# Kernel tuning notes

Hardware: AMD Instinct MI355X
Metric: run time of the kernel (lower is better)

The kernel has to match this reference:

```python
import jax, jax.numpy as jnp
import numpy as np

B, N, D_MODEL = 4, 4096, 1024
HEADS, DIM_HEAD = 8, 64
INNER = HEADS * DIM_HEAD  # 512
NB_FEAT = int(DIM_HEAD * np.log(DIM_HEAD))  # 266, performer default
D_FF = 4 * D_MODEL
KERNEL_EPS = 1e-4
LN_EPS = 1e-5


def setup_inputs() -> dict:
    key = jax.random.key(0)
    ks = jax.random.split(key, 12)
    w = lambda i, shape: jax.random.normal(ks[i], shape, jnp.float32) * 0.02
    z = lambda *shape: jnp.zeros(shape, jnp.float32)
    o = lambda *shape: jnp.ones(shape, jnp.float32)
    return dict(
        x=jax.random.normal(ks[0], (B, N, D_MODEL), jnp.float32),
        proj_w=w(1, (D_MODEL, D_MODEL)), proj_b=z(D_MODEL),
        ln1_g=o(D_MODEL), ln1_b=z(D_MODEL),
        wq=w(2, (D_MODEL, INNER)), bq=z(INNER),
        wk=w(3, (D_MODEL, INNER)), bk=z(INNER),
        wv=w(4, (D_MODEL, INNER)), bv=z(INNER),
        wo=w(5, (INNER, D_MODEL)), bo=z(D_MODEL),
        proj_mat=jax.random.normal(ks[6], (NB_FEAT, DIM_HEAD), jnp.float32),
        ln2_g=o(D_MODEL), ln2_b=z(D_MODEL),
        w1=w(7, (D_MODEL, D_FF)), b1=z(D_FF),
        w2=w(8, (D_FF, D_MODEL)), b2=z(D_MODEL),
    )


def _layer_norm(x, g, b):
    mu = x.mean(-1, keepdims=True)
    var = ((x - mu) ** 2).mean(-1, keepdims=True)
    return (x - mu) * jax.lax.rsqrt(var + LN_EPS) * g + b


def _softmax_kernel(data, proj_mat, is_query):
    # data: [b,h,n,d], proj_mat: [m,d] -> features [b,h,n,m]
    dn = DIM_HEAD ** -0.25            # data_normalizer
    ratio = NB_FEAT ** -0.5
    dd = jnp.einsum('bhnd,md->bhnm', data * dn, proj_mat)
    diag = (data ** 2).sum(-1, keepdims=True) * (0.5 * dn * dn)
    if is_query:
        mx = dd.max(-1, keepdims=True)
    else:
        mx = dd.max(axis=(-1, -2), keepdims=True)
    return ratio * (jnp.exp(dd - diag - mx) + KERNEL_EPS)


def _favor_attention(q, k, v, proj_mat):
    # non-causal FAVOR+ linear attention; q,k,v: [b,h,n,d]
    qp = _softmax_kernel(q, proj_mat, True)    # [b,h,n,m]
    kp = _softmax_kernel(k, proj_mat, False)   # [b,h,n,m]
    k_sum = kp.sum(-2)                         # [b,h,m]
    d_inv = 1.0 / jnp.einsum('bhnm,bhm->bhn', qp, k_sum)
    ctx = jnp.einsum('bhnm,bhnd->bhmd', kp, v)
    return jnp.einsum('bhmd,bhnm,bhn->bhnd', ctx, qp, d_inv)


def _performer(x, ln1_g, ln1_b, wq, bq, wk, bk, wv, bv, wo, bo, proj_mat,
               ln2_g, ln2_b, w1, b1, w2, b2):
    # pre-norm self-attention block
    h = _layer_norm(x, ln1_g, ln1_b)
    split = lambda t: t.reshape(B, N, HEADS, DIM_HEAD).transpose(0, 2, 1, 3)
    q = split(h @ wq + bq)
    k = split(h @ wk + bk)
    v = split(h @ wv + bv)
    attn = _favor_attention(q, k, v, proj_mat)
    attn = attn.transpose(0, 2, 1, 3).reshape(B, N, INNER)
    x = x + attn @ wo + bo
    # pre-norm feed-forward block
    h = _layer_norm(x, ln2_g, ln2_b)
    x = x + jax.nn.gelu(h @ w1 + b1, approximate=False) @ w2 + b2
    return x


def reference(x, proj_w, proj_b, ln1_g, ln1_b, wq, bq, wk, bk, wv, bv,
              wo, bo, proj_mat, ln2_g, ln2_b, w1, b1, w2, b2):
    u = x @ proj_w + proj_b                    # dense gate branch
    v = _performer(x, ln1_g, ln1_b, wq, bq, wk, bk, wv, bv, wo, bo,
                   proj_mat, ln2_g, ln2_b, w1, b1, w2, b2)
    return u * v
```

## Files before the change

kernel.cpp:

```cpp
#include <hip/hip_runtime.h>
#include <math.h>

typedef unsigned short bf16_t;
using bf16x8 = __attribute__((ext_vector_type(8))) short;
using f32x4  = __attribute__((ext_vector_type(4))) float;

#define DEVFN static __device__ __forceinline__

DEVFN float b2f(bf16_t u){ unsigned v=((unsigned)u)<<16; float f; __builtin_memcpy(&f,&v,4); return f; }
DEVFN bf16_t f2b(float f){ unsigned u; __builtin_memcpy(&u,&f,4); u += 0x7fffu + ((u>>16)&1u); return (bf16_t)(u>>16); }
DEVFN unsigned encf(float f){ unsigned u=__float_as_uint(f); return (u&0x80000000u)? ~u : (u|0x80000000u); }
DEVFN float decf(unsigned e){ return __uint_as_float((e&0x80000000u)? (e^0x80000000u) : ~e); }

DEVFN float erf_fast(float x){
  float ax = fabsf(x);
  float t = __builtin_amdgcn_rcpf(1.0f + 0.3275911f*ax);
  float y = t*(0.254829592f + t*(-0.284496736f + t*(1.421413741f
          + t*(-1.453152027f + t*1.061405429f))));
  float r = 1.0f - y*__expf(-ax*ax);
  return copysignf(r, x);
}

constexpr float DN_SCALE = 0.35355339059327373f;
constexpr float RATIO    = 0.06131393394849658f;
constexpr float KEPS     = 1e-4f;
#define MPAD 288

#define GLOAD_LDS16(g, l) __builtin_amdgcn_global_load_lds( \
    (__attribute__((address_space(1))) void*)(g), \
    (__attribute__((address_space(3))) void*)(l), 16, 0, 0)

#define MFMA16(a,b,c) __builtin_amdgcn_mfma_f32_16x16x32_bf16(a,b,c,0,0,0)

DEVFN void hard_barrier(){
  __builtin_amdgcn_sched_barrier(0);
  asm volatile("s_barrier" ::: "memory");
  __builtin_amdgcn_sched_barrier(0);
}
#define WAITVM(N) asm volatile("s_waitcnt vmcnt(" #N ")" ::: "memory")

__global__ __launch_bounds__(256)
void wt_cast(const float* __restrict__ W, bf16_t* __restrict__ Wt, int K, int N)
{
  __shared__ alignas(16) float ts[32][33];
  int t = threadIdx.x;
  int r = t>>3, c4 = (t&7)*4;
  int k0 = blockIdx.x*32, n0 = blockIdx.y*32;
  float4 v = *(const float4*)(W + (size_t)(k0+r)*N + n0 + c4);
  ts[r][c4+0]=v.x; ts[r][c4+1]=v.y; ts[r][c4+2]=v.z; ts[r][c4+3]=v.w;
  __syncthreads();
  ushort4 o;
  o.x = f2b(ts[c4+0][r]); o.y = f2b(ts[c4+1][r]);
  o.z = f2b(ts[c4+2][r]); o.w = f2b(ts[c4+3][r]);
  *(ushort4*)(Wt + (size_t)(n0+r)*K + k0 + c4) = o;
}

__global__ __launch_bounds__(256)
void concat_bias(const float* __restrict__ bq, const float* __restrict__ bk,
                 const float* __restrict__ bv, float* __restrict__ dst)
{
  int t = blockIdx.x*256 + threadIdx.x;
  if (t < 512) dst[t] = bq[t];
  else if (t < 1024) dst[t] = bk[t-512];
  else dst[t] = bv[t-1024];
}

__global__ void mx_init(unsigned* m){ if (threadIdx.x < 32) m[threadIdx.x] = 0u; }

__global__ void zero_out(float* o, long n){
  long i = (long)blockIdx.x*256 + threadIdx.x;
  if (i < n) o[i] = 0.f;
}

__global__ __launch_bounds__(256)
void pm_cast(const float* __restrict__ pm, bf16_t* __restrict__ pmb)
{
  int idx = blockIdx.x*256 + threadIdx.x;
  int r = idx>>6, c = idx&63;
  pmb[idx] = (r < 266) ? f2b(pm[r*64+c]*DN_SCALE) : (bf16_t)0;
}

__global__ __launch_bounds__(256)
void vt_trans(const bf16_t* __restrict__ qkv, bf16_t* __restrict__ vT)
{
  __shared__ ushort ts[32][36];
  int by = blockIdx.y;
  int bh = by>>1, dt = by&1, b = bh>>3, h = bh&7;
  int n0 = blockIdx.x*32;
  int t = threadIdx.x, r = t>>3, c4 = (t&7)*4;
  ushort4 v = *(const ushort4*)(qkv + ((size_t)b*4096 + n0 + r)*1536 + 1024 + h*64 + dt*32 + c4);
  ts[r][c4+0]=v.x; ts[r][c4+1]=v.y; ts[r][c4+2]=v.z; ts[r][c4+3]=v.w;
  __syncthreads();
  ushort4 o;
  o.x = ts[c4+0][r]; o.y = ts[c4+1][r]; o.z = ts[c4+2][r]; o.w = ts[c4+3][r];
  *(ushort4*)(vT + ((size_t)bh*64 + dt*32 + r)*4096 + n0 + c4) = o;
}

__global__ __launch_bounds__(256)
void ln_kernel(const float* __restrict__ x, const float* __restrict__ g,
               const float* __restrict__ b, bf16_t* __restrict__ out)
{
  long row = blockIdx.x; int t = threadIdx.x;
  float4 v = ((const float4*)x)[row*256 + t];
  float s = v.x+v.y+v.z+v.w;
  #pragma unroll
  for (int o=32;o>0;o>>=1) s += __shfl_xor(s, o);
  __shared__ float r1[4], r2[4];
  if ((t&63)==0) r1[t>>6] = s;
  __syncthreads();
  float mu = (r1[0]+r1[1]+r1[2]+r1[3]) * (1.f/1024.f);
  float dx = v.x-mu, dy = v.y-mu, dz = v.z-mu, dw = v.w-mu;
  float ss = dx*dx+dy*dy+dz*dz+dw*dw;
  #pragma unroll
  for (int o=32;o>0;o>>=1) ss += __shfl_xor(ss, o);
  if ((t&63)==0) r2[t>>6] = ss;
  __syncthreads();
  float var = (r2[0]+r2[1]+r2[2]+r2[3]) * (1.f/1024.f);
  float rs = rsqrtf(var + 1e-5f);
  float4 gg = ((const float4*)g)[t], bb = ((const float4*)b)[t];
  ushort4 o4;
  o4.x = f2b(dx*rs*gg.x+bb.x); o4.y = f2b(dy*rs*gg.y+bb.y);
  o4.z = f2b(dz*rs*gg.z+bb.z); o4.w = f2b(dw*rs*gg.w+bb.w);
  ((ushort4*)out)[row*256+t] = o4;
}

__global__ __launch_bounds__(256)
void cast_f32_bf16(const float* __restrict__ in, bf16_t* __restrict__ out)
{
  long i = (long)blockIdx.x*256 + threadIdx.x;
  float4 v = ((const float4*)in)[i];
  ushort4 o;
  o.x = f2b(v.x); o.y = f2b(v.y); o.z = f2b(v.z); o.w = f2b(v.w);
  ((ushort4*)out)[i] = o;
}

template<int RES, int GELU, int GATEF, int OBF>
__global__ __launch_bounds__(256)
void gemm_bt(const bf16_t* __restrict__ A, int lda,
             const bf16_t* __restrict__ Bt, int ldb,
             const float* __restrict__ bias,
             const float* res,
             const float* gatef,
             void* Cout, int N, int K)
{
  __shared__ alignas(16) bf16_t As[3][128*32];
  __shared__ alignas(16) bf16_t Bs[3][128*32];
  const int tid = threadIdx.x;
  const int wid = tid>>6, lane = tid&63;
  const int l15 = lane&15, l4 = lane>>4;
  const int wm = wid>>1, wn = wid&1;

  const int NX = gridDim.x;
  const int nwg = NX * gridDim.y;
  const int lid = blockIdx.y*NX + blockIdx.x;
  const int qc = nwg>>3;
  const int wgid = (lid&7)*qc + (lid>>3);
  const int stripe = wgid / (16*NX);
  const int rem    = wgid % (16*NX);
  const long m0 = (long)(stripe*16 + (rem & 15))*128;
  const long n0 = (long)(rem >> 4)*128;

  f32x4 acc[4][4];
  #pragma unroll
  for (int i=0;i<4;i++)
    #pragma unroll
    for (int j=0;j<4;j++) acc[i][j] = f32x4{0.f,0.f,0.f,0.f};

  const bf16_t* ga = A  + (size_t)(m0 + (tid>>2))*lda + (tid&3)*8;
  const bf16_t* gb = Bt + (size_t)(n0 + (tid>>2))*ldb + (tid&3)*8;

  auto STAGE = [&](bf16_t* Ab, bf16_t* Bb){
    GLOAD_LDS16(ga,                   Ab + wid*512);
    GLOAD_LDS16(ga + (size_t)64*lda,  Ab + 2048 + wid*512);
    GLOAD_LDS16(gb,                   Bb + wid*512);
    GLOAD_LDS16(gb + (size_t)64*ldb,  Bb + 2048 + wid*512);
    ga += 32; gb += 32;
  };

  const int nt = K >> 5;
  STAGE(As[0], Bs[0]);
  STAGE(As[1], Bs[1]);
  int i0 = 0, i1 = 1, i2 = 2;
  for (int t = 0; t < nt; ++t){
    if (t+2 < nt){ STAGE(As[i2], Bs[i2]); WAITVM(8); }
    else if (t+1 < nt){ WAITVM(4); }
    else { WAITVM(0); }
    hard_barrier();
    const bf16_t* Ab = As[i0];
    const bf16_t* Bb = Bs[i0];
    bf16x8 af[4], bfr[4];
    #pragma unroll
    for (int i=0;i<4;i++){
      af[i]  = *(const bf16x8*)(Ab + (wm*64 + i*16 + l15)*32 + l4*8);
      bfr[i] = *(const bf16x8*)(Bb + (wn*64 + i*16 + l15)*32 + l4*8);
    }
    #pragma unroll
    for (int i=0;i<4;i++)
      #pragma unroll
      for (int j=0;j<4;j++)
        acc[i][j] = MFMA16(af[i], bfr[j], acc[i][j]);
    hard_barrier();
    int tmp = i0; i0 = i1; i1 = i2; i2 = tmp;
  }

  #pragma unroll
  for (int i=0;i<4;i++){
    #pragma unroll
    for (int j=0;j<4;j++){
      #pragma unroll
      for (int r=0;r<4;r++){
        long row = m0 + wm*64 + i*16 + l4*4 + r;
        long col = n0 + wn*64 + j*16 + l15;
        float v = acc[i][j][r] + bias[col];
        if constexpr (RES)   v += res[row*(long)N + col];
        if constexpr (GELU)  v = 0.5f*v*(1.0f + erf_fast(v*0.70710678118654752f));
        if constexpr (GATEF) v *= gatef[row*(long)N + col];
        if constexpr (OBF)  ((bf16_t*)Cout)[row*(long)N + col] = f2b(v);
        else                ((float* )Cout)[row*(long)N + col] = v;
      }
    }
  }
}


__global__ __launch_bounds__(256,2)
void favor_kmax2(const bf16_t* __restrict__ qkv, const bf16_t* __restrict__ pmb,
                 unsigned* __restrict__ mxk)
{
  int bh = blockIdx.y, b = bh>>3, h = bh&7;
  int t = threadIdx.x, wid = t>>6, lane = t&63;
  int l15 = lane&15, l4 = lane>>4;
  int n0 = blockIdx.x*64, row0 = wid*16;
  f32x4 acc[18];
  #pragma unroll
  for (int c=0;c<18;c++) acc[c] = f32x4{0.f,0.f,0.f,0.f};
  const bf16_t* abase = qkv + ((size_t)(b*4096) + n0 + row0 + l15)*1536 + 512 + h*64;
  #pragma unroll
  for (int kh=0;kh<2;kh++){
    bf16x8 a = *(const bf16x8*)(abase + kh*32 + l4*8);
    #pragma unroll
    for (int ct=0;ct<18;ct++){
      bf16x8 bb = *(const bf16x8*)(pmb + (ct*16+l15)*64 + kh*32 + l4*8);
      acc[ct] = MFMA16(a, bb, acc[ct]);
    }
  }
  float mx = -3e38f;
  #pragma unroll
  for (int ct=0;ct<18;ct++){
    if (ct*16 + l15 < 266){
      #pragma unroll
      for (int r=0;r<4;r++) mx = fmaxf(mx, acc[ct][r]);
    }
  }
  #pragma unroll
  for (int o=32;o>0;o>>=1) mx = fmaxf(mx, __shfl_xor(mx, o));
  __shared__ float red[4];
  if (lane==0) red[wid] = mx;
  __syncthreads();
  if (t==0){
    float m2 = fmaxf(fmaxf(red[0],red[1]),fmaxf(red[2],red[3]));
    atomicMax(mxk + bh, encf(m2));
  }
}

__global__ __launch_bounds__(256,2)
void favor_kp(const bf16_t* __restrict__ qkv, const bf16_t* __restrict__ pmb,
              const unsigned* __restrict__ mxk, bf16_t* __restrict__ kpT, int bh0)
{
  int bhl = blockIdx.y, bh = bh0 + bhl, b = bh>>3, h = bh&7;
  int t = threadIdx.x, wid = t>>6, lane = t&63;
  int l15 = lane&15, l4 = lane>>4;
  int n0 = blockIdx.x*64, row0 = wid*16;
  f32x4 acc[18];
  #pragma unroll
  for (int c=0;c<18;c++) acc[c] = f32x4{0.f,0.f,0.f,0.f};
  const bf16_t* abase = qkv + ((size_t)(b*4096) + n0 + row0 + l15)*1536 + 512 + h*64;
  float rsq = 0.f;
  #pragma unroll
  for (int kh=0;kh<2;kh++){
    bf16x8 a = *(const bf16x8*)(abase + kh*32 + l4*8);
    #pragma unroll
    for (int e=0;e<8;e++){ float v = b2f((bf16_t)a[e]); rsq += v*v; }
    #pragma unroll
    for (int ct=0;ct<18;ct++){
      bf16x8 bb = *(const bf16x8*)(pmb + (ct*16+l15)*64 + kh*32 + l4*8);
      acc[ct] = MFMA16(a, bb, acc[ct]);
    }
  }
  rsq += __shfl_xor(rsq, 16);
  rsq += __shfl_xor(rsq, 32);
  float MX = decf(mxk[bh]);
  constexpr float DSC = 0.5f*DN_SCALE*DN_SCALE;
  float dg[4];
  #pragma unroll
  for (int r=0;r<4;r++) dg[r] = DSC * __shfl(rsq, l4*4 + r);
  #pragma unroll
  for (int ct=0;ct<18;ct++){
    int col = ct*16 + l15;
    ushort4 o;
    if (col < 266){
      o.x = f2b(RATIO*(__expf(acc[ct][0] - dg[0] - MX) + KEPS));
      o.y = f2b(RATIO*(__expf(acc[ct][1] - dg[1] - MX) + KEPS));
      o.z = f2b(RATIO*(__expf(acc[ct][2] - dg[2] - MX) + KEPS));
      o.w = f2b(RATIO*(__expf(acc[ct][3] - dg[3] - MX) + KEPS));
    } else { o.x=0; o.y=0; o.z=0; o.w=0; }
    *(ushort4*)(kpT + ((size_t)bhl*MPAD + col)*4096 + n0 + row0 + l4*4) = o;
  }
}

__global__ __launch_bounds__(256)
void ksum_kernel(const bf16_t* __restrict__ kpT, float* __restrict__ ksumf, int bh0)
{
  int t = threadIdx.x, wid = t>>6, lane = t&63;
  int rr = blockIdx.x*4 + wid;
  int bhl = rr/272, m = rr%272;
  const bf16_t* row = kpT + ((size_t)bhl*MPAD + m)*4096;
  float s = 0.f;
  #pragma unroll
  for (int j=0;j<8;j++){
    bf16x8 v = *(const bf16x8*)(row + j*512 + lane*8);
    #pragma unroll
    for (int e=0;e<8;e++) s += b2f((bf16_t)v[e]);
  }
  #pragma unroll
  for (int o=32;o>0;o>>=1) s += __shfl_xor(s, o);
  if (lane==0) ksumf[(size_t)(bh0+bhl)*MPAD + m] = s;
}

__global__ __launch_bounds__(256,2)
void ctx_gemm(const bf16_t* __restrict__ kpT, const bf16_t* __restrict__ vT,
              float* __restrict__ ctxP, int bh0)
{
  int m0 = blockIdx.x*16, ks = blockIdx.y, bhl = blockIdx.z, bh = bh0 + bhl;
  int t = threadIdx.x, wid = t>>6, lane = t&63;
  int l15 = lane&15, l4 = lane>>4;
  f32x4 acc[4];
  #pragma unroll
  for (int c=0;c<4;c++) acc[c] = f32x4{0.f,0.f,0.f,0.f};
  const bf16_t* Abase = kpT + ((size_t)bhl*MPAD + m0 + l15)*4096;
  const bf16_t* Bbase = vT + ((size_t)bh*64)*4096;
  const int kb = ks*1024 + wid*256;
  for (int k = kb; k < kb + 256; k += 32){
    bf16x8 a = *(const bf16x8*)(Abase + k + l4*8);
    #pragma unroll
    for (int ct=0;ct<4;ct++){
      bf16x8 bb = *(const bf16x8*)(Bbase + (size_t)(ct*16+l15)*4096 + k + l4*8);
      acc[ct] = MFMA16(a, bb, acc[ct]);
    }
  }
  __shared__ float red[4][4][16][16];
  #pragma unroll
  for (int ct=0;ct<4;ct++)
    #pragma unroll
    for (int r=0;r<4;r++) red[wid][ct][l4*4+r][l15] = acc[ct][r];
  __syncthreads();
  #pragma unroll
  for (int i=0;i<4;i++){
    int e = i*256 + t;
    int ct = e>>8, row = (e>>4)&15, col = e&15;
    float s = ((red[0][ct][row][col] + red[1][ct][row][col])
             + (red[2][ct][row][col] + red[3][ct][row][col]));
    ctxP[(((size_t)bhl*4 + ks)*272 + m0 + row)*64 + ct*16 + col] = s;
  }
}

__global__ __launch_bounds__(256)
void ctx_reduce(const float* __restrict__ ctxP, bf16_t* __restrict__ ctxT, int bh0)
{
  int bhl = blockIdx.y, bh = bh0 + bhl;
  int idx = blockIdx.x*256 + threadIdx.x;
  int m = idx>>6, d = idx&63;
  float s = 0.f;
  if (m < 272){
    #pragma unroll
    for (int ks=0;ks<4;ks++)
      s += ctxP[(((size_t)bhl*4 + ks)*272 + m)*64 + d];
  }
  ctxT[((size_t)bh*64 + d)*MPAD + m] = f2b(s);
}

__global__ __launch_bounds__(256,2)
void favor_q(const bf16_t* __restrict__ qkv, const bf16_t* __restrict__ pmb,
             const float* __restrict__ ksumf,
             const bf16_t* __restrict__ ctxT, bf16_t* __restrict__ attn)
{
  __shared__ alignas(16) ushort qpLds[64*296];
  __shared__ float ksLds[288];
  int bh = blockIdx.y, b = bh>>3, h = bh&7;
  int t = threadIdx.x, wid = t>>6, lane = t&63;
  int l15 = lane&15, l4 = lane>>4;
  int n0 = blockIdx.x*64, row0 = wid*16;
  ksLds[t] = ksumf[(size_t)bh*MPAD + t];
  if (t < 32) ksLds[256+t] = ksumf[(size_t)bh*MPAD + 256 + t];
  __syncthreads();

  f32x4 acc[18];
  #pragma unroll
  for (int c=0;c<18;c++) acc[c] = f32x4{0.f,0.f,0.f,0.f};
  const bf16_t* abase = qkv + ((size_t)(b*4096) + n0 + row0 + l15)*1536 + h*64;
  float rsq = 0.f;
  #pragma unroll
  for (int kh=0;kh<2;kh++){
    bf16x8 a = *(const bf16x8*)(abase + kh*32 + l4*8);
    #pragma unroll
    for (int e=0;e<8;e++){ float v = b2f((bf16_t)a[e]); rsq += v*v; }
    #pragma unroll
    for (int ct=0;ct<18;ct++){
      bf16x8 bb = *(const bf16x8*)(pmb + (ct*16+l15)*64 + kh*32 + l4*8);
      acc[ct] = MFMA16(a, bb, acc[ct]);
    }
  }
  rsq += __shfl_xor(rsq, 16);
  rsq += __shfl_xor(rsq, 32);
  constexpr float DSC = 0.5f*DN_SCALE*DN_SCALE;
  float dg[4];
  #pragma unroll
  for (int r=0;r<4;r++) dg[r] = DSC * __shfl(rsq, l4*4 + r);

  float mxr[4] = {-3e38f,-3e38f,-3e38f,-3e38f};
  #pragma unroll
  for (int ct=0;ct<18;ct++){
    if (ct*16 + l15 < 266){
      #pragma unroll
      for (int r=0;r<4;r++) mxr[r] = fmaxf(mxr[r], acc[ct][r]);
    }
  }
  #pragma unroll
  for (int r=0;r<4;r++){
    mxr[r] = fmaxf(mxr[r], __shfl_xor(mxr[r], 1));
    mxr[r] = fmaxf(mxr[r], __shfl_xor(mxr[r], 2));
    mxr[r] = fmaxf(mxr[r], __shfl_xor(mxr[r], 4));
    mxr[r] = fmaxf(mxr[r], __shfl_xor(mxr[r], 8));
  }
  float den[4] = {0.f,0.f,0.f,0.f};
  #pragma unroll
  for (int ct=0;ct<18;ct++){
    int col = ct*16 + l15;
    float ks = ksLds[col];
    #pragma unroll
    for (int r=0;r<4;r++){
      float qpv = 0.f;
      if (col < 266){
        qpv = RATIO*(__expf(acc[ct][r] - dg[r] - mxr[r]) + KEPS);
        den[r] += qpv*ks;
      }
      qpLds[(row0 + l4*4 + r)*296 + col] = f2b(qpv);
    }
  }
  float dinv[4];
  #pragma unroll
  for (int r=0;r<4;r++){
    den[r] += __shfl_xor(den[r], 1);
    den[r] += __shfl_xor(den[r], 2);
    den[r] += __shfl_xor(den[r], 4);
    den[r] += __shfl_xor(den[r], 8);
    dinv[r] = 1.0f/den[r];
  }
  __syncthreads();

  f32x4 o2[4];
  #pragma unroll
  for (int c=0;c<4;c++) o2[c] = f32x4{0.f,0.f,0.f,0.f};
  const bf16_t* Bbase = ctxT + (size_t)bh*64*MPAD;
  #pragma unroll
  for (int kk=0;kk<9;kk++){
    int k0 = kk*32;
    bf16x8 a = *(const bf16x8*)&qpLds[(row0 + l15)*296 + k0 + l4*8];
    #pragma unroll
    for (int ct=0;ct<4;ct++){
      bf16x8 bb = *(const bf16x8*)(Bbase + (size_t)(ct*16+l15)*MPAD + k0 + l4*8);
      o2[ct] = MFMA16(a, bb, o2[ct]);
    }
  }
  #pragma unroll
  for (int ct=0;ct<4;ct++)
    #pragma unroll
    for (int r=0;r<4;r++)
      attn[((size_t)(b*4096) + n0 + row0 + l4*4 + r)*512 + h*64 + ct*16 + l15]
        = f2b(o2[ct][r] * dinv[r]);
}

extern "C" void kernel_launch(void* const* d_in, const int* in_sizes, int n_in,
                              void* d_out, int out_size, void* d_ws, size_t ws_size,
                              hipStream_t stream)
{
  (void)in_sizes; (void)n_in; (void)out_size;
  const float* x      = (const float*)d_in[0];
  const float* proj_w = (const float*)d_in[1];
  const float* proj_b = (const float*)d_in[2];
  const float* ln1_g  = (const float*)d_in[3];
  const float* ln1_b  = (const float*)d_in[4];
  const float* wq     = (const float*)d_in[5];
  const float* bq     = (const float*)d_in[6];
  const float* wk     = (const float*)d_in[7];
  const float* bk     = (const float*)d_in[8];
  const float* wv     = (const float*)d_in[9];
  const float* bv     = (const float*)d_in[10];
  const float* wo     = (const float*)d_in[11];
  const float* bo     = (const float*)d_in[12];
  const float* pm     = (const float*)d_in[13];
  const float* ln2_g  = (const float*)d_in[14];
  const float* ln2_b  = (const float*)d_in[15];
  const float* w1     = (const float*)d_in[16];
  const float* b1     = (const float*)d_in[17];
  const float* w2     = (const float*)d_in[18];
  const float* b2     = (const float*)d_in[19];
  float* out = (float*)d_out;
  const size_t MB = 1ull<<20;

  char* ws = (char*)d_ws;
  size_t off = 0;
  auto alloc = [&](size_t bytes)->void*{ void* p = ws + off; off += (bytes + 255) & ~(size_t)255; return p; };
  bf16_t* Wt_proj = (bf16_t*)alloc(2ul*1024*1024);
  bf16_t* Wt_qkv  = (bf16_t*)alloc(2ul*1536*1024);
  bf16_t* Wt_o    = (bf16_t*)alloc(2ul*1024*512);
  bf16_t* Wt_1    = (bf16_t*)alloc(2ul*4096*1024);
  bf16_t* Wt_2    = (bf16_t*)alloc(2ul*1024*4096);
  float*  bqkv    = (float*) alloc(4ul*1536);
  unsigned* mxk   = (unsigned*)alloc(4ul*32);
  bf16_t* pmb     = (bf16_t*)alloc(2ul*MPAD*64);
  float*  ksumf   = (float*) alloc(4ul*32*MPAD);
  bf16_t* ctxT    = (bf16_t*)alloc(2ul*32*64*MPAD);
  float*  ctxP    = (float*) alloc(4ul*8*4*272*64);
  char*   R       = (char*)  alloc(0);
  size_t R_avail = (ws_size > off) ? ws_size - off : 0;

  if (R_avail < 67*MB){ zero_out<<<dim3(65536), 256, 0, stream>>>(out, 16777216L); return; }
  int KG = (R_avail >= 87*MB) ? 8 : 4;
  int NC = (R_avail >= 84*MB) ? 2 : 4;

  bf16_t* qkv  = (bf16_t*)(R);
  bf16_t* h1c  = (bf16_t*)(R + 48*MB);
  bf16_t* kpT  = (bf16_t*)(R + 48*MB);
  bf16_t* attn = (bf16_t*)(R + 48*MB);
  long    CH   = 16384/NC;
  bf16_t* h2c  = (bf16_t*)(R);
  bf16_t* ff1c = (bf16_t*)(R + 16*MB);
  bf16_t* vT   = (bf16_t*)d_out;

  wt_cast<<<dim3(32,32), 256, 0, stream>>>(proj_w, Wt_proj, 1024, 1024);
  wt_cast<<<dim3(32,16), 256, 0, stream>>>(wq, Wt_qkv,              1024, 512);
  wt_cast<<<dim3(32,16), 256, 0, stream>>>(wk, Wt_qkv + 512*1024,   1024, 512);
  wt_cast<<<dim3(32,16), 256, 0, stream>>>(wv, Wt_qkv + 1024*1024,  1024, 512);
  wt_cast<<<dim3(16,32), 256, 0, stream>>>(wo, Wt_o, 512, 1024);
  wt_cast<<<dim3(32,128),256, 0, stream>>>(w1, Wt_1, 1024, 4096);
  wt_cast<<<dim3(128,32),256, 0, stream>>>(w2, Wt_2, 4096, 1024);
  concat_bias<<<dim3(6), 256, 0, stream>>>(bq, bk, bv, bqkv);
  pm_cast<<<dim3(72), 256, 0, stream>>>(pm, pmb);

  for (int c = 0; c < 2; c++){
    ln_kernel<<<dim3(8192), 256, 0, stream>>>(x + (size_t)c*8192*1024, ln1_g, ln1_b, h1c);
    gemm_bt<0,0,0,1><<<dim3(12,64), 256, 0, stream>>>(h1c, 1024, Wt_qkv, 1024,
        bqkv, nullptr, nullptr, qkv + (size_t)c*8192*1536, 1536, 1024);
  }

  vt_trans<<<dim3(128,64), 256, 0, stream>>>(qkv, vT);
  mx_init<<<dim3(1), 64, 0, stream>>>(mxk);
  favor_kmax2<<<dim3(64,32), 256, 0, stream>>>(qkv, pmb, mxk);
  for (int g = 0; g < 32; g += KG){
    favor_kp<<<dim3(64,KG), 256, 0, stream>>>(qkv, pmb, mxk, kpT, g);
    ksum_kernel<<<dim3(KG*68), 256, 0, stream>>>(kpT, ksumf, g);
    ctx_gemm<<<dim3(17,4,KG), 256, 0, stream>>>(kpT, vT, ctxP, g);
    ctx_reduce<<<dim3(72,KG), 256, 0, stream>>>(ctxP, ctxT, g);
  }
  favor_q<<<dim3(64,32), 256, 0, stream>>>(qkv, pmb, ksumf, ctxT, attn);

  gemm_bt<1,0,0,0><<<dim3(8,128), 256, 0, stream>>>(attn, 512, Wt_o, 512,
      bo, x, nullptr, out, 1024, 512);

  for (int c = 0; c < NC; c++){
    float* xrow = out + (size_t)c*CH*1024;
    ln_kernel<<<dim3((unsigned)CH), 256, 0, stream>>>(xrow, ln2_g, ln2_b, h2c);
    gemm_bt<0,1,0,1><<<dim3(32,(unsigned)(CH/128)), 256, 0, stream>>>(h2c, 1024, Wt_1, 1024,
        b1, nullptr, nullptr, ff1c, 4096, 1024);
    gemm_bt<1,0,0,0><<<dim3(8,(unsigned)(CH/128)), 256, 0, stream>>>(ff1c, 4096, Wt_2, 4096,
        b2, xrow, nullptr, xrow, 1024, 4096);
    cast_f32_bf16<<<dim3((unsigned)CH), 256, 0, stream>>>(x + (size_t)c*CH*1024, h2c);
    gemm_bt<0,0,1,0><<<dim3(8,(unsigned)(CH/128)), 256, 0, stream>>>(h2c, 1024, Wt_proj, 1024,
        proj_b, nullptr, xrow, xrow, 1024, 1024);
  }
}
```

Baseline: 1.032 ms.

## Fuse k_sum into ctx_gemm and use one barrier per GEMM k-step

Removes the separate ksum_kernel by accumulating the per-feature sums of the bf16 kp rows inside ctx_gemm as the A fragments are loaded, then reducing the partial sums in ctx_reduce. This saves one extra read of kpT and a kernel launch per group. It also changes the GEMM main loop to wait and barrier once per step, issuing the next stage's async loads after that barrier instead of before it. Dropping the trailing barrier relies on the triple-buffer rotation to avoid overwriting LDS that other waves are still reading. The favor_q load of ksumf now guards against entries past 272.

Result: no change. 1.020 ms (-1.1%).

```diff
diff --git a/kernel.cpp b/kernel.cpp
--- a/kernel.cpp
+++ b/kernel.cpp
@@ -32,12 +32,8 @@
 
 #define MFMA16(a,b,c) __builtin_amdgcn_mfma_f32_16x16x32_bf16(a,b,c,0,0,0)
 
-DEVFN void hard_barrier(){
-  __builtin_amdgcn_sched_barrier(0);
-  asm volatile("s_barrier" ::: "memory");
-  __builtin_amdgcn_sched_barrier(0);
-}
 #define WAITVM(N) asm volatile("s_waitcnt vmcnt(" #N ")" ::: "memory")
+#define RAW_BARRIER() asm volatile("s_barrier" ::: "memory")
 
 __global__ __launch_bounds__(256)
 void wt_cast(const float* __restrict__ W, bf16_t* __restrict__ Wt, int K, int N)
@@ -182,10 +178,10 @@
   STAGE(As[1], Bs[1]);
   int i0 = 0, i1 = 1, i2 = 2;
   for (int t = 0; t < nt; ++t){
-    if (t+2 < nt){ STAGE(As[i2], Bs[i2]); WAITVM(8); }
-    else if (t+1 < nt){ WAITVM(4); }
-    else { WAITVM(0); }
-    hard_barrier();
+    if (t < nt-1) { WAITVM(4); }
+    else          { WAITVM(0); }
+    RAW_BARRIER();
+    if (t+2 < nt) STAGE(As[i2], Bs[i2]);
     const bf16_t* Ab = As[i0];
     const bf16_t* Bb = Bs[i0];
     bf16x8 af[4], bfr[4];
@@ -199,7 +195,6 @@
       #pragma unroll
       for (int j=0;j<4;j++)
         acc[i][j] = MFMA16(af[i], bfr[j], acc[i][j]);
-    hard_barrier();
     int tmp = i0; i0 = i1; i1 = i2; i2 = tmp;
   }
 
@@ -308,28 +303,9 @@
   }
 }
 
-__global__ __launch_bounds__(256)
-void ksum_kernel(const bf16_t* __restrict__ kpT, float* __restrict__ ksumf, int bh0)
-{
-  int t = threadIdx.x, wid = t>>6, lane = t&63;
-  int rr = blockIdx.x*4 + wid;
-  int bhl = rr/272, m = rr%272;
-  const bf16_t* row = kpT + ((size_t)bhl*MPAD + m)*4096;
-  float s = 0.f;
-  #pragma unroll
-  for (int j=0;j<8;j++){
-    bf16x8 v = *(const bf16x8*)(row + j*512 + lane*8);
-    #pragma unroll
-    for (int e=0;e<8;e++) s += b2f((bf16_t)v[e]);
-  }
-  #pragma unroll
-  for (int o=32;o>0;o>>=1) s += __shfl_xor(s, o);
-  if (lane==0) ksumf[(size_t)(bh0+bhl)*MPAD + m] = s;
-}
-
 __global__ __launch_bounds__(256,2)
 void ctx_gemm(const bf16_t* __restrict__ kpT, const bf16_t* __restrict__ vT,
-              float* __restrict__ ctxP, int bh0)
+              float* __restrict__ ctxP, float* __restrict__ ksumP, int bh0)
 {
   int m0 = blockIdx.x*16, ks = blockIdx.y, bhl = blockIdx.z, bh = bh0 + bhl;
   int t = threadIdx.x, wid = t>>6, lane = t&63;
@@ -340,15 +316,22 @@
   const bf16_t* Abase = kpT + ((size_t)bhl*MPAD + m0 + l15)*4096;
   const bf16_t* Bbase = vT + ((size_t)bh*64)*4096;
   const int kb = ks*1024 + wid*256;
+  float ksp = 0.f;
   for (int k = kb; k < kb + 256; k += 32){
     bf16x8 a = *(const bf16x8*)(Abase + k + l4*8);
+    #pragma unroll
+    for (int e=0;e<8;e++) ksp += b2f((bf16_t)a[e]);
     #pragma unroll
     for (int ct=0;ct<4;ct++){
       bf16x8 bb = *(const bf16x8*)(Bbase + (size_t)(ct*16+l15)*4096 + k + l4*8);
       acc[ct] = MFMA16(a, bb, acc[ct]);
     }
   }
+  ksp += __shfl_xor(ksp, 16);
+  ksp += __shfl_xor(ksp, 32);
   __shared__ float red[4][4][16][16];
+  __shared__ float ksred[4][16];
+  if (l4 == 0) ksred[wid][l15] = ksp;
   #pragma unroll
   for (int ct=0;ct<4;ct++)
     #pragma unroll
@@ -362,10 +345,15 @@
              + (red[2][ct][row][col] + red[3][ct][row][col]));
     ctxP[(((size_t)bhl*4 + ks)*272 + m0 + row)*64 + ct*16 + col] = s;
   }
-}
-
-__global__ __launch_bounds__(256)
-void ctx_reduce(const float* __restrict__ ctxP, bf16_t* __restrict__ ctxT, int bh0)
+  if (t < 16){
+    float s2 = ksred[0][t] + ksred[1][t] + ksred[2][t] + ksred[3][t];
+    ksumP[((size_t)bhl*4 + ks)*272 + m0 + t] = s2;
+  }
+}
+
+__global__ __launch_bounds__(256)
+void ctx_reduce(const float* __restrict__ ctxP, const float* __restrict__ ksumP,
+                bf16_t* __restrict__ ctxT, float* __restrict__ ksumf, int bh0)
 {
   int bhl = blockIdx.y, bh = bh0 + bhl;
   int idx = blockIdx.x*256 + threadIdx.x;
@@ -377,6 +365,13 @@
       s += ctxP[(((size_t)bhl*4 + ks)*272 + m)*64 + d];
   }
   ctxT[((size_t)bh*64 + d)*MPAD + m] = f2b(s);
+  if (idx < 272){
+    float s2 = 0.f;
+    #pragma unroll
+    for (int ks=0;ks<4;ks++)
+      s2 += ksumP[(((size_t)bhl*4 + ks)*272) + idx];
+    ksumf[(size_t)bh*MPAD + idx] = s2;
+  }
 }
 
 __global__ __launch_bounds__(256,2)
@@ -390,8 +385,8 @@
   int t = threadIdx.x, wid = t>>6, lane = t&63;
   int l15 = lane&15, l4 = lane>>4;
   int n0 = blockIdx.x*64, row0 = wid*16;
-  ksLds[t] = ksumf[(size_t)bh*MPAD + t];
-  if (t < 32) ksLds[256+t] = ksumf[(size_t)bh*MPAD + 256 + t];
+  ksLds[t] = (t < 272) ? ksumf[(size_t)bh*MPAD + t] : 0.f;
+  if (t < 32) ksLds[256+t] = (256+t < 272) ? ksumf[(size_t)bh*MPAD + 256 + t] : 0.f;
   __syncthreads();
 
   f32x4 acc[18];
@@ -522,6 +517,7 @@
   float*  ksumf   = (float*) alloc(4ul*32*MPAD);
   bf16_t* ctxT    = (bf16_t*)alloc(2ul*32*64*MPAD);
   float*  ctxP    = (float*) alloc(4ul*8*4*272*64);
+  float*  ksumP   = (float*) alloc(4ul*8*4*272);
   char*   R       = (char*)  alloc(0);
   size_t R_avail = (ws_size > off) ? ws_size - off : 0;
 
@@ -559,9 +555,8 @@
   favor_kmax2<<<dim3(64,32), 256, 0, stream>>>(qkv, pmb, mxk);
   for (int g = 0; g < 32; g += KG){
     favor_kp<<<dim3(64,KG), 256, 0, stream>>>(qkv, pmb, mxk, kpT, g);
-    ksum_kernel<<<dim3(KG*68), 256, 0, stream>>>(kpT, ksumf, g);
-    ctx_gemm<<<dim3(17,4,KG), 256, 0, stream>>>(kpT, vT, ctxP, g);
-    ctx_reduce<<<dim3(72,KG), 256, 0, stream>>>(ctxP, ctxT, g);
+    ctx_gemm<<<dim3(17,4,KG), 256, 0, stream>>>(kpT, vT, ctxP, ksumP, g);
+    ctx_reduce<<<dim3(72,KG), 256, 0, stream>>>(ctxP, ksumP, ctxT, ksumf, g);
   }
   favor_q<<<dim3(64,32), 256, 0, stream>>>(qkv, pmb, ksumf, ctxT, attn);
 
```
